# Kernel tuning notes

Hardware: AMD Instinct MI355X
Metric: run time of the kernel (lower is better)

## Reference

```python
import jax, jax.numpy as jnp
import numpy as np
import math

B, C, H, W = 16, 256, 56, 56
NH, WS = 8, 7            # num_heads, window_size
HID = 1024               # mlp_ratio * C

def _gelu(x):
    return jax.nn.gelu(x, approximate=False)  # torch nn.GELU default (erf)

def _ln(x, w, b, eps=1e-6):
    m = jnp.mean(x, -1, keepdims=True)
    v = jnp.mean((x - m) ** 2, -1, keepdims=True)
    return (x - m) * jax.lax.rsqrt(v + eps) * w + b

def _bn(x, g, b, eps=1e-5):
    # training-mode BatchNorm2d: batch statistics over (N,H,W)
    m = jnp.mean(x, (0, 2, 3), keepdims=True)
    v = jnp.mean((x - m) ** 2, (0, 2, 3), keepdims=True)
    return (x - m) * jax.lax.rsqrt(v + eps) * g[None, :, None, None] + b[None, :, None, None]

def _dwconv(x, w, b=None):
    y = jax.lax.conv_general_dilated(x, w, (1, 1), 'SAME',
                                     feature_group_count=x.shape[1],
                                     dimension_numbers=('NCHW', 'OIHW', 'NCHW'))
    if b is not None:
        y = y + b[None, :, None, None]
    return y

def _rel_pos_index(Wh, Ww):
    seq1 = np.arange(Wh) * (2 * Ww - 1)
    seq2 = np.arange(Ww)
    coords = (seq1[:, None] + seq2[None, :]).reshape(1, -1)
    idx = coords + coords.T               # [Wh*Ww, Wh*Ww]
    return jnp.asarray(np.ascontiguousarray(idx[:, ::-1]))  # flip(1)

REL_IDX = _rel_pos_index(WS, WS)  # [49, 49]

def setup_inputs():
    key = jax.random.key(0)
    ks = jax.random.split(key, 10)
    s = 0.02
    return dict(
        x=jax.random.normal(ks[0], (B, C, H, W), jnp.float32),
        ln1_w=jnp.ones((C,), jnp.float32), ln1_b=jnp.zeros((C,), jnp.float32),
        pos_w1=jax.random.normal(ks[1], (C, 1, 3, 3), jnp.float32) * s,
        pos_w2=jax.random.normal(ks[2], (C, 1, 3, 3), jnp.float32) * s,
        qkv_w=jax.random.normal(ks[3], (3 * C, C), jnp.float32) * s,
        qkv_b=jnp.zeros((3 * C,), jnp.float32),
        rpb=jax.random.normal(ks[4], ((2 * WS - 1) ** 2, NH), jnp.float32) * s,
        proj_w=jax.random.normal(ks[5], (C, C), jnp.float32) * s,
        proj_b=jnp.zeros((C,), jnp.float32),
        ln2_w=jnp.ones((C,), jnp.float32), ln2_b=jnp.zeros((C,), jnp.float32),
        fc1_w=jax.random.normal(ks[6], (HID, C), jnp.float32) * s,
        fc1_b=jnp.zeros((HID,), jnp.float32),
        bn1_g=jnp.ones((HID,), jnp.float32), bn1_b=jnp.zeros((HID,), jnp.float32),
        dw_w=jax.random.normal(ks[7], (HID, 1, 3, 3), jnp.float32) * s,
        dw_b=jnp.zeros((HID,), jnp.float32),
        bn2_g=jnp.ones((HID,), jnp.float32), bn2_b=jnp.zeros((HID,), jnp.float32),
        fc2_w=jax.random.normal(ks[8], (C, HID), jnp.float32) * s,
        fc2_b=jnp.zeros((C,), jnp.float32),
        bn3_g=jnp.ones((C,), jnp.float32), bn3_b=jnp.zeros((C,), jnp.float32),
    )

def _attention(xl, Hh, Ww_, pos_w1, pos_w2, qkv_w, qkv_b, rpb, proj_w, proj_b):
    Bq, N, Cc = xl.shape
    Wh = Ww = WS
    Hp = math.ceil(Hh / Wh) * Wh
    Wp = math.ceil(Ww_ / Ww) * Ww
    ph, pw = Hp - Hh, Wp - Ww_
    y = xl.reshape(Bq, Hh, Ww_, Cc)
    if ph or pw:
        y = jnp.pad(y, ((0, 0), (ph // 2, ph - ph // 2), (pw // 2, pw - pw // 2), (0, 0)))
    nWh, nWw = Hp // Wh, Wp // Ww
    # window partition -> [B*nWh*nWw, C, Wh, Ww]
    y = y.reshape(Bq, nWh, Wh, nWw, Ww, Cc).transpose(0, 1, 3, 2, 4, 5)
    xw = y.reshape(-1, Wh, Ww, Cc).transpose(0, 3, 1, 2)
    # per-window depthwise positional embedding: dw3x3 -> GELU -> dw3x3
    xw = xw + _dwconv(_gelu(_dwconv(xw, pos_w1)), pos_w2)
    t = xw.transpose(0, 2, 3, 1).reshape(-1, Wh * Ww, Cc)  # [Bw, 49, C]
    hd = Cc // NH
    qkv = (t @ qkv_w.T + qkv_b).reshape(-1, Wh * Ww, 3, NH, hd).transpose(2, 0, 3, 1, 4)
    q, k, v = qkv[0] * (hd ** -0.5), qkv[1], qkv[2]        # [Bw, NH, 49, hd]
    attn = jnp.einsum('bhnd,bhmd->bhnm', q, k)
    bias = rpb[REL_IDX.reshape(-1)].reshape(Wh * Ww, Wh * Ww, NH).transpose(2, 0, 1)
    attn = jax.nn.softmax(attn + bias[None], axis=-1)
    o = jnp.einsum('bhnm,bhmd->bhnd', attn, v).transpose(0, 2, 1, 3).reshape(-1, Wh * Ww, Cc)
    o = o @ proj_w.T + proj_b
    # window merge + crop padding
    o = o.reshape(Bq, nWh, nWw, Wh, Ww, Cc).transpose(0, 1, 3, 2, 4, 5).reshape(Bq, Hp, Wp, Cc)
    o = o[:, ph // 2:Hh + ph // 2, pw // 2:Ww_ + pw // 2]
    return o.reshape(Bq, N, Cc)

def _ffn(z_nlc, Hh, Ww_, fc1_w, fc1_b, bn1_g, bn1_b, dw_w, dw_b, bn2_g, bn2_b,
         fc2_w, fc2_b, bn3_g, bn3_b):
    Bq, N, Cc = z_nlc.shape
    z = z_nlc.transpose(0, 2, 1).reshape(Bq, Cc, Hh, Ww_)
    z = jnp.einsum('bchw,oc->bohw', z, fc1_w) + fc1_b[None, :, None, None]
    z = _gelu(_bn(z, bn1_g, bn1_b))
    z = _gelu(_bn(_dwconv(z, dw_w, dw_b), bn2_g, bn2_b))
    z = jnp.einsum('bchw,oc->bohw', z, fc2_w) + fc2_b[None, :, None, None]
    z = _gelu(_bn(z, bn3_g, bn3_b))
    return z.reshape(Bq, z.shape[1], Hh * Ww_).transpose(0, 2, 1)

def reference(x, ln1_w, ln1_b, pos_w1, pos_w2, qkv_w, qkv_b, rpb, proj_w, proj_b,
              ln2_w, ln2_b, fc1_w, fc1_b, bn1_g, bn1_b, dw_w, dw_b, bn2_g, bn2_b,
              fc2_w, fc2_b, bn3_g, bn3_b):
    Bq, Cc, Hh, Ww_ = x.shape
    xl = x.reshape(Bq, Cc, Hh * Ww_).transpose(0, 2, 1)  # NCHW -> NLC
    xl = xl + _attention(_ln(xl, ln1_w, ln1_b), Hh, Ww_,
                         pos_w1, pos_w2, qkv_w, qkv_b, rpb, proj_w, proj_b)
    xl = xl + _ffn(_ln(xl, ln2_w, ln2_b), Hh, Ww_,
                   fc1_w, fc1_b, bn1_g, bn1_b, dw_w, dw_b, bn2_g, bn2_b,
                   fc2_w, fc2_b, bn3_g, bn3_b)
    return xl.transpose(0, 2, 1).reshape(Bq, Cc, Hh, Ww_)
```

## Files before the change

kernel.cpp:

```cpp
#include <hip/hip_runtime.h>
#include <math.h>

#define BB 16
#define CC 256
#define HH 56
#define WW2 56
#define HWW 3136
#define NTOK 50176
#define NHD 8
#define HD 32
#define WSZ 7
#define WIN 49
#define NWIN 1024
#define HID 1024
#define C3 768

typedef __attribute__((ext_vector_type(8))) short bf16x8;
typedef __attribute__((ext_vector_type(4))) float f32x4;

__device__ __forceinline__ float gelu_f(float x) {
    return 0.5f * x * (1.0f + erff(x * 0.70710678118654752f));
}

__global__ __launch_bounds__(256) void k_nchw_to_tok(const float* __restrict__ x,
                                                     float* __restrict__ xl) {
    __shared__ float tile[32][33];
    int b = blockIdx.z;
    int p0 = blockIdx.x * 32, c0 = blockIdx.y * 32;
    int tx = threadIdx.x, ty = threadIdx.y;
    const float* xb = x + (size_t)b * CC * HWW;
    #pragma unroll
    for (int r = 0; r < 32; r += 8)
        tile[ty + r][tx] = xb[(size_t)(c0 + ty + r) * HWW + p0 + tx];
    __syncthreads();
    float* xlb = xl + (size_t)b * HWW * CC;
    #pragma unroll
    for (int r = 0; r < 32; r += 8)
        xlb[(size_t)(p0 + ty + r) * CC + c0 + tx] = tile[tx][ty + r];
}

__global__ __launch_bounds__(256) void k_tok_to_nchw(const float* __restrict__ zl,
                                                     float* __restrict__ out) {
    __shared__ float tile[32][33];
    int b = blockIdx.z;
    int p0 = blockIdx.x * 32, c0 = blockIdx.y * 32;
    int tx = threadIdx.x, ty = threadIdx.y;
    const float* zb = zl + (size_t)b * HWW * CC;
    #pragma unroll
    for (int r = 0; r < 32; r += 8)
        tile[ty + r][tx] = zb[(size_t)(p0 + ty + r) * CC + c0 + tx];
    __syncthreads();
    float* ob = out + (size_t)b * CC * HWW;
    #pragma unroll
    for (int r = 0; r < 32; r += 8)
        ob[(size_t)(c0 + ty + r) * HWW + p0 + tx] = tile[tx][ty + r];
}

__global__ __launch_bounds__(256) void k_ln(const float* __restrict__ in,
                                            const float* __restrict__ w,
                                            const float* __restrict__ bia,
                                            float* __restrict__ out) {
    size_t t = blockIdx.x;
    int c = threadIdx.x;
    float v = in[t * CC + c];
    float s = v, sq = v * v;
    #pragma unroll
    for (int off = 32; off; off >>= 1) {
        s += __shfl_xor(s, off);
        sq += __shfl_xor(sq, off);
    }
    __shared__ float red[8];
    int wid = c >> 6, lane = c & 63;
    if (lane == 0) { red[wid] = s; red[4 + wid] = sq; }
    __syncthreads();
    s = red[0] + red[1] + red[2] + red[3];
    sq = red[4] + red[5] + red[6] + red[7];
    float m = s * (1.0f / CC);
    float var = sq * (1.0f / CC) - m * m;
    float rs = rsqrtf(var + 1e-6f);
    out[t * CC + c] = (v - m) * rs * w[c] + bia[c];
}

__global__ __launch_bounds__(256) void k_posenc(const float* __restrict__ xln,
                                                const float* __restrict__ w1,
                                                const float* __restrict__ w2,
                                                float* __restrict__ tout) {
    int win = blockIdx.x;
    int c = threadIdx.x;
    int b = win >> 6, wh = (win >> 3) & 7, ww = win & 7;
    const float* base = xln + ((size_t)b * HWW) * CC + c;
    float v[49];
    #pragma unroll
    for (int r = 0; r < 7; r++)
        #pragma unroll
        for (int s = 0; s < 7; s++)
            v[r * 7 + s] = base[(size_t)((wh * 7 + r) * WW2 + ww * 7 + s) * CC];
    float k1w[9], k2w[9];
    #pragma unroll
    for (int k = 0; k < 9; k++) { k1w[k] = w1[c * 9 + k]; k2w[k] = w2[c * 9 + k]; }
    float g[49];
    #pragma unroll
    for (int r = 0; r < 7; r++)
        #pragma unroll
        for (int s = 0; s < 7; s++) {
            float acc = 0.f;
            #pragma unroll
            for (int kr = 0; kr < 3; kr++)
                #pragma unroll
                for (int ks = 0; ks < 3; ks++) {
                    int rr = r + kr - 1, ss = s + ks - 1;
                    if (rr >= 0 && rr < 7 && ss >= 0 && ss < 7)
                        acc += v[rr * 7 + ss] * k1w[kr * 3 + ks];
                }
            g[r * 7 + s] = gelu_f(acc);
        }
    float* outp = tout + (size_t)win * WIN * CC + c;
    #pragma unroll
    for (int r = 0; r < 7; r++)
        #pragma unroll
        for (int s = 0; s < 7; s++) {
            float acc = 0.f;
            #pragma unroll
            for (int kr = 0; kr < 3; kr++)
                #pragma unroll
                for (int ks = 0; ks < 3; ks++) {
                    int rr = r + kr - 1, ss = s + ks - 1;
                    if (rr >= 0 && rr < 7 && ss >= 0 && ss < 7)
                        acc += g[rr * 7 + ss] * k2w[kr * 3 + ks];
                }
            outp[(size_t)(r * 7 + s) * CC] = v[r * 7 + s] + acc;
        }
}

__device__ __forceinline__ void cvt_split4(float4 v, unsigned& h0, unsigned& h1,
                                           unsigned& l0, unsigned& l1) {
    unsigned ux = __float_as_uint(v.x), uy = __float_as_uint(v.y);
    unsigned uz = __float_as_uint(v.z), uw = __float_as_uint(v.w);
    unsigned hx = ux & 0xFFFF0000u, hy = uy & 0xFFFF0000u;
    unsigned hz = uz & 0xFFFF0000u, hw = uw & 0xFFFF0000u;
    float lx = v.x - __uint_as_float(hx);
    float ly = v.y - __uint_as_float(hy);
    float lz = v.z - __uint_as_float(hz);
    float lw = v.w - __uint_as_float(hw);
    h0 = (hx >> 16) | hy;
    h1 = (hz >> 16) | hw;
    l0 = (__float_as_uint(lx) >> 16) | (__float_as_uint(ly) & 0xFFFF0000u);
    l1 = (__float_as_uint(lz) >> 16) | (__float_as_uint(lw) & 0xFFFF0000u);
}

#define LDK 40
template <int EPI>
__global__ __launch_bounds__(256) void k_gemm_mfma(const float* __restrict__ A,
                                                   const float* __restrict__ Bw,
                                                   const float* __restrict__ bias,
                                                   float* __restrict__ Out,
                                                   float* __restrict__ resid,
                                                   int N, int K) {
    __shared__ __align__(16) unsigned short Ah[128 * LDK];
    __shared__ __align__(16) unsigned short Al[128 * LDK];
    __shared__ __align__(16) unsigned short Bh[128 * LDK];
    __shared__ __align__(16) unsigned short Bl[128 * LDK];
    const int tid = threadIdx.x;
    const int bm = blockIdx.y * 128;
    const int bn = blockIdx.x * 128;
    const int srow = tid >> 3;
    const int skf = (tid & 7) * 4;
    const int lane = tid & 63;
    const int wave = tid >> 6;
    const int wm = (wave & 1) * 64;
    const int wn = (wave >> 1) * 64;
    const int frow = lane & 15;
    const int fk = (lane >> 4) * 8;

    f32x4 acc[4][4] = {};

    for (int k0 = 0; k0 < K; k0 += 32) {
        if (k0) __syncthreads();
        #pragma unroll
        for (int h = 0; h < 4; ++h) {
            int row = srow + h * 32;
            float4 av = *reinterpret_cast<const float4*>(&A[(size_t)(bm + row) * K + k0 + skf]);
            float4 bv = *reinterpret_cast<const float4*>(&Bw[(size_t)(bn + row) * K + k0 + skf]);
            unsigned h0, h1, l0, l1;
            cvt_split4(av, h0, h1, l0, l1);
            *reinterpret_cast<uint2*>(&Ah[row * LDK + skf]) = make_uint2(h0, h1);
            *reinterpret_cast<uint2*>(&Al[row * LDK + skf]) = make_uint2(l0, l1);
            cvt_split4(bv, h0, h1, l0, l1);
            *reinterpret_cast<uint2*>(&Bh[row * LDK + skf]) = make_uint2(h0, h1);
            *reinterpret_cast<uint2*>(&Bl[row * LDK + skf]) = make_uint2(l0, l1);
        }
        __syncthreads();
        bf16x8 a_h[4], a_l[4], b_h[4], b_l[4];
        #pragma unroll
        for (int mi = 0; mi < 4; mi++) {
            int idx = (wm + mi * 16 + frow) * LDK + fk;
            a_h[mi] = *reinterpret_cast<const bf16x8*>(&Ah[idx]);
            a_l[mi] = *reinterpret_cast<const bf16x8*>(&Al[idx]);
        }
        #pragma unroll
        for (int nj = 0; nj < 4; nj++) {
            int idx = (wn + nj * 16 + frow) * LDK + fk;
            b_h[nj] = *reinterpret_cast<const bf16x8*>(&Bh[idx]);
            b_l[nj] = *reinterpret_cast<const bf16x8*>(&Bl[idx]);
        }
        #pragma unroll
        for (int mi = 0; mi < 4; mi++)
            #pragma unroll
            for (int nj = 0; nj < 4; nj++) {
                acc[mi][nj] = __builtin_amdgcn_mfma_f32_16x16x32_bf16(a_h[mi], b_h[nj], acc[mi][nj], 0, 0, 0);
                acc[mi][nj] = __builtin_amdgcn_mfma_f32_16x16x32_bf16(a_l[mi], b_h[nj], acc[mi][nj], 0, 0, 0);
                acc[mi][nj] = __builtin_amdgcn_mfma_f32_16x16x32_bf16(a_h[mi], b_l[nj], acc[mi][nj], 0, 0, 0);
            }
    }

    const int rbase = (lane >> 4) * 4;
    #pragma unroll
    for (int mi = 0; mi < 4; mi++) {
        #pragma unroll
        for (int nj = 0; nj < 4; nj++) {
            int gcol = bn + wn + nj * 16 + frow;
            float bval = bias[gcol];
            #pragma unroll
            for (int r = 0; r < 4; r++) {
                int grow = bm + wm + mi * 16 + rbase + r;
                float val = acc[mi][nj][r] + bval;
                if (EPI == 0) {
                    Out[(size_t)grow * N + gcol] = val;
                } else {
                    int win = grow / 49, ii = grow - win * 49;
                    int b = win >> 6, wh = (win >> 3) & 7, ww = win & 7;
                    int rr = ii / 7, ss = ii - rr * 7;
                    size_t tok = (size_t)b * HWW + (size_t)((wh * 7 + rr) * WW2 + ww * 7 + ss);
                    resid[tok * CC + gcol] += val;
                }
            }
        }
    }
}

__global__ __launch_bounds__(256) void k_attn(const float* __restrict__ qkv,
                                              const float* __restrict__ rpb,
                                              float* __restrict__ O) {
    __shared__ float qs[49][32], ks[49][32], vs[49][32];
    __shared__ float S[49][52];
    const int tid = threadIdx.x;
    const int win = blockIdx.x >> 3;
    const int head = blockIdx.x & 7;
    const float* base = qkv + (size_t)win * WIN * C3 + head * HD;
    for (int idx = tid; idx < WIN * HD; idx += 256) {
        int i = idx >> 5, d = idx & 31;
        const float* bp = base + (size_t)i * C3 + d;
        qs[i][d] = bp[0] * 0.17677669529663687f;
        ks[i][d] = bp[CC];
        vs[i][d] = bp[2 * CC];
    }
    __syncthreads();
    for (int idx = tid; idx < WIN * WIN; idx += 256) {
        int i = idx / 49, j = idx - i * 49;
        const float4* qp = reinterpret_cast<const float4*>(qs[i]);
        const float4* kp = reinterpret_cast<const float4*>(ks[j]);
        float acc = 0.f;
        #pragma unroll
        for (int d = 0; d < 8; d++) {
            float4 a = qp[d], b2 = kp[d];
            acc += a.x * b2.x + a.y * b2.y + a.z * b2.z + a.w * b2.w;
        }
        int ci = (i / 7) * 13 + (i % 7);
        int jr = 48 - j;
        int cj = (jr / 7) * 13 + (jr % 7);
        S[i][j] = acc + rpb[(ci + cj) * NHD + head];
    }
    __syncthreads();
    int wid = tid >> 6, lane = tid & 63;
    for (int row = wid; row < 49; row += 4) {
        float v = (lane < 49) ? S[row][lane] : -1e30f;
        float mx = v;
        #pragma unroll
        for (int off = 32; off; off >>= 1) mx = fmaxf(mx, __shfl_xor(mx, off));
        float e = (lane < 49) ? __expf(v - mx) : 0.f;
        float sm = e;
        #pragma unroll
        for (int off = 32; off; off >>= 1) sm += __shfl_xor(sm, off);
        if (lane < 49) S[row][lane] = e / sm;
    }
    __syncthreads();
    float* ob = O + (size_t)win * WIN * CC + head * HD;
    for (int idx = tid; idx < WIN * HD; idx += 256) {
        int i = idx >> 5, d = idx & 31;
        float acc = 0.f;
        #pragma unroll
        for (int j = 0; j < 49; j++) acc += S[i][j] * vs[j][d];
        ob[(size_t)i * CC + d] = acc;
    }
}

__global__ __launch_bounds__(256) void k_colstats(const float* __restrict__ Z,
                                                  float* __restrict__ sums, int nch) {
    int c = blockIdx.y * 256 + threadIdx.x;
    int t0 = blockIdx.x * 256;
    const float* zp = Z + (size_t)t0 * nch + c;
    float s = 0.f, sq = 0.f;
    for (int t = 0; t < 256; t++) {
        float v = zp[(size_t)t * nch];
        s += v; sq += v * v;
    }
    atomicAdd(&sums[c], s);
    atomicAdd(&sums[nch + c], sq);
}

__global__ void k_bnfin(const float* __restrict__ sums, const float* __restrict__ g,
                        const float* __restrict__ b, float* __restrict__ ss, int nch) {
    int c = blockIdx.x * 256 + threadIdx.x;
    if (c >= nch) return;
    float m = sums[c] * (1.0f / NTOK);
    float var = sums[nch + c] * (1.0f / NTOK) - m * m;
    float sc = rsqrtf(var + 1e-5f) * g[c];
    ss[c] = sc;
    ss[nch + c] = b[c] - m * sc;
}

__global__ __launch_bounds__(256) void k_act(float* __restrict__ Z,
                                             const float* __restrict__ ss,
                                             int nch, size_t total4) {
    size_t idx = (size_t)blockIdx.x * 256 + threadIdx.x;
    if (idx >= total4) return;
    float4 v = reinterpret_cast<float4*>(Z)[idx];
    int c0 = (int)((idx << 2) & (size_t)(nch - 1));
    v.x = gelu_f(v.x * ss[c0 + 0] + ss[nch + c0 + 0]);
    v.y = gelu_f(v.y * ss[c0 + 1] + ss[nch + c0 + 1]);
    v.z = gelu_f(v.z * ss[c0 + 2] + ss[nch + c0 + 2]);
    v.w = gelu_f(v.w * ss[c0 + 3] + ss[nch + c0 + 3]);
    reinterpret_cast<float4*>(Z)[idx] = v;
}

__global__ __launch_bounds__(256) void k_resfin(float* __restrict__ Z,
                                                const float* __restrict__ XL,
                                                const float* __restrict__ ss,
                                                size_t total4) {
    size_t idx = (size_t)blockIdx.x * 256 + threadIdx.x;
    if (idx >= total4) return;
    float4 v = reinterpret_cast<float4*>(Z)[idx];
    float4 xr = reinterpret_cast<const float4*>(XL)[idx];
    int c0 = (int)((idx << 2) & (size_t)(CC - 1));
    v.x = gelu_f(v.x * ss[c0 + 0] + ss[CC + c0 + 0]) + xr.x;
    v.y = gelu_f(v.y * ss[c0 + 1] + ss[CC + c0 + 1]) + xr.y;
    v.z = gelu_f(v.z * ss[c0 + 2] + ss[CC + c0 + 2]) + xr.z;
    v.w = gelu_f(v.w * ss[c0 + 3] + ss[CC + c0 + 3]) + xr.w;
    reinterpret_cast<float4*>(Z)[idx] = v;
}

__global__ __launch_bounds__(256) void k_dwconv_ip(float* __restrict__ Z,
                                                   const float* __restrict__ wt,
                                                   const float* __restrict__ bias) {
    __shared__ float rb[3][56][32];
    const int b  = blockIdx.x >> 5;
    const int c0 = (blockIdx.x & 31) * 32;
    const int tid = threadIdx.x;
    const int c = tid & 31, wg = tid >> 5;
    float* zb = Z + (size_t)b * HWW * HID + c0;
    float w9[9];
    #pragma unroll
    for (int k = 0; k < 9; k++) w9[k] = wt[(c0 + c) * 9 + k];
    const float bval = bias[c0 + c];

    for (int idx = tid; idx < 56 * 32; idx += 256) {
        int wcol = idx >> 5, ch = idx & 31;
        rb[0][wcol][ch] = zb[(size_t)(0 * 56 + wcol) * HID + ch];
        rb[1][wcol][ch] = zb[(size_t)(1 * 56 + wcol) * HID + ch];
    }
    __syncthreads();

    for (int h = 0; h < 56; ++h) {
        const int bm1 = (h + 2) % 3;
        const int b0  = h % 3;
        const int bp1 = (h + 1) % 3;
        float outv[7];
        #pragma unroll
        for (int i = 0; i < 7; i++) {
            int w = wg * 7 + i;
            float acc = bval;
            #pragma unroll
            for (int kr = 0; kr < 3; kr++) {
                int hh = h + kr - 1;
                if (hh < 0 || hh >= 56) continue;
                const float (*row)[32] = (kr == 0) ? rb[bm1] : (kr == 1 ? rb[b0] : rb[bp1]);
                #pragma unroll
                for (int ks = 0; ks < 3; ks++) {
                    int ww = w + ks - 1;
                    if (ww < 0 || ww >= 56) continue;
                    acc += row[ww][c] * w9[kr * 3 + ks];
                }
            }
            outv[i] = acc;
        }
        #pragma unroll
        for (int i = 0; i < 7; i++)
            zb[(size_t)(h * 56 + wg * 7 + i) * HID + c] = outv[i];
        __syncthreads();
        if (h + 2 < 56) {
            for (int idx = tid; idx < 56 * 32; idx += 256) {
                int wcol = idx >> 5, ch = idx & 31;
                rb[bm1][wcol][ch] = zb[(size_t)((h + 2) * 56 + wcol) * HID + ch];
            }
        }
        __syncthreads();
    }
}

__global__ __launch_bounds__(256) void k_zero(float* __restrict__ p, size_t n) {
    size_t i = (size_t)blockIdx.x * 256 + threadIdx.x;
    if (i < n) p[i] = 0.f;
}

extern "C" void kernel_launch(void* const* d_in, const int* in_sizes, int n_in,
                              void* d_out, int out_size, void* d_ws, size_t ws_size,
                              hipStream_t stream) {
    const float* x      = (const float*)d_in[0];
    const float* ln1_w  = (const float*)d_in[1];
    const float* ln1_b  = (const float*)d_in[2];
    const float* pos_w1 = (const float*)d_in[3];
    const float* pos_w2 = (const float*)d_in[4];
    const float* qkv_w  = (const float*)d_in[5];
    const float* qkv_b  = (const float*)d_in[6];
    const float* rpb    = (const float*)d_in[7];
    const float* proj_w = (const float*)d_in[8];
    const float* proj_b = (const float*)d_in[9];
    const float* ln2_w  = (const float*)d_in[10];
    const float* ln2_b  = (const float*)d_in[11];
    const float* fc1_w  = (const float*)d_in[12];
    const float* fc1_b  = (const float*)d_in[13];
    const float* bn1_g  = (const float*)d_in[14];
    const float* bn1_b  = (const float*)d_in[15];
    const float* dw_w   = (const float*)d_in[16];
    const float* dw_b   = (const float*)d_in[17];
    const float* bn2_g  = (const float*)d_in[18];
    const float* bn2_b  = (const float*)d_in[19];
    const float* fc2_w  = (const float*)d_in[20];
    const float* fc2_b  = (const float*)d_in[21];
    const float* bn3_g  = (const float*)d_in[22];
    const float* bn3_b  = (const float*)d_in[23];
    float* OUT = (float*)d_out;

    const size_t SMALL = (size_t)NTOK * CC;
    const size_t BIG   = (size_t)NTOK * HID;
    const size_t QKVF  = (size_t)NTOK * C3;
    const size_t NEED  = (SMALL + BIG + 8 * HID) * sizeof(float);

    if (ws_size < NEED) {
        k_zero<<<(unsigned)((SMALL + 255) / 256), 256, 0, stream>>>(OUT, SMALL);
        return;
    }

    float* ws = (float*)d_ws;
    float* XL   = ws;
    float* BIGR = XL + SMALL;
    float* SCR  = BIGR + QKVF;
    float* SUMS = BIGR + BIG;
    float* SS1  = SUMS + 2 * HID;
    float* SS2  = SS1 + 2 * HID;
    float* SS3  = SS2 + 2 * HID;

    dim3 tb(32, 8);
    dim3 tg(HWW / 32, CC / 32, BB);

    k_nchw_to_tok<<<tg, tb, 0, stream>>>(x, XL);
    k_ln<<<NTOK, 256, 0, stream>>>(XL, ln1_w, ln1_b, OUT);
    k_posenc<<<NWIN, 256, 0, stream>>>(OUT, pos_w1, pos_w2, SCR);
    k_gemm_mfma<0><<<dim3(C3 / 128, NTOK / 128), 256, 0, stream>>>(SCR, qkv_w, qkv_b, BIGR, nullptr, C3, CC);
    k_attn<<<NWIN * NHD, 256, 0, stream>>>(BIGR, rpb, OUT);
    k_gemm_mfma<1><<<dim3(CC / 128, NTOK / 128), 256, 0, stream>>>(OUT, proj_w, proj_b, nullptr, XL, CC, CC);
    k_ln<<<NTOK, 256, 0, stream>>>(XL, ln2_w, ln2_b, OUT);
    k_gemm_mfma<0><<<dim3(HID / 128, NTOK / 128), 256, 0, stream>>>(OUT, fc1_w, fc1_b, BIGR, nullptr, HID, CC);
    hipMemsetAsync(SUMS, 0, 2 * HID * sizeof(float), stream);
    k_colstats<<<dim3(NTOK / 256, HID / 256), 256, 0, stream>>>(BIGR, SUMS, HID);
    k_bnfin<<<HID / 256, 256, 0, stream>>>(SUMS, bn1_g, bn1_b, SS1, HID);
    k_act<<<(unsigned)(BIG / 4 / 256), 256, 0, stream>>>(BIGR, SS1, HID, BIG / 4);
    k_dwconv_ip<<<BB * 32, 256, 0, stream>>>(BIGR, dw_w, dw_b);
    hipMemsetAsync(SUMS, 0, 2 * HID * sizeof(float), stream);
    k_colstats<<<dim3(NTOK / 256, HID / 256), 256, 0, stream>>>(BIGR, SUMS, HID);
    k_bnfin<<<HID / 256, 256, 0, stream>>>(SUMS, bn2_g, bn2_b, SS2, HID);
    k_act<<<(unsigned)(BIG / 4 / 256), 256, 0, stream>>>(BIGR, SS2, HID, BIG / 4);
    k_gemm_mfma<0><<<dim3(CC / 128, NTOK / 128), 256, 0, stream>>>(BIGR, fc2_w, fc2_b, OUT, nullptr, CC, HID);
    hipMemsetAsync(SUMS, 0, 2 * CC * sizeof(float), stream);
    k_colstats<<<dim3(NTOK / 256, CC / 256), 256, 0, stream>>>(OUT, SUMS, CC);
    k_bnfin<<<1, 256, 0, stream>>>(SUMS, bn3_g, bn3_b, SS3, CC);
    k_resfin<<<(unsigned)(SMALL / 4 / 256), 256, 0, stream>>>(OUT, XL, SS3, SMALL / 4);
    k_tok_to_nchw<<<tg, tb, 0, stream>>>(OUT, XL);
    hipMemcpyAsync(OUT, XL, SMALL * sizeof(float), hipMemcpyDeviceToDevice, stream);
}
```

Measured before the change: 1.583 ms.

## Store FFN hidden activations in bf16 and fuse BN/GELU into dwconv and fc2 loads

```diff
diff --git a/kernel.cpp b/kernel.cpp
--- a/kernel.cpp
+++ b/kernel.cpp
@@ -17,9 +17,18 @@
 
 typedef __attribute__((ext_vector_type(8))) short bf16x8;
 typedef __attribute__((ext_vector_type(4))) float f32x4;
+typedef unsigned short u16;
 
 __device__ __forceinline__ float gelu_f(float x) {
     return 0.5f * x * (1.0f + erff(x * 0.70710678118654752f));
+}
+__device__ __forceinline__ float bf2f(u16 u) {
+    return __uint_as_float(((unsigned)u) << 16);
+}
+__device__ __forceinline__ u16 f2bf(float f) {
+    unsigned u = __float_as_uint(f);
+    u += 0x7FFFu + ((u >> 16) & 1u);
+    return (u16)(u >> 16);
 }
 
 __global__ __launch_bounds__(256) void k_nchw_to_tok(const float* __restrict__ x,
@@ -37,23 +46,6 @@
     #pragma unroll
     for (int r = 0; r < 32; r += 8)
         xlb[(size_t)(p0 + ty + r) * CC + c0 + tx] = tile[tx][ty + r];
-}
-
-__global__ __launch_bounds__(256) void k_tok_to_nchw(const float* __restrict__ zl,
-                                                     float* __restrict__ out) {
-    __shared__ float tile[32][33];
-    int b = blockIdx.z;
-    int p0 = blockIdx.x * 32, c0 = blockIdx.y * 32;
-    int tx = threadIdx.x, ty = threadIdx.y;
-    const float* zb = zl + (size_t)b * HWW * CC;
-    #pragma unroll
-    for (int r = 0; r < 32; r += 8)
-        tile[ty + r][tx] = zb[(size_t)(p0 + ty + r) * CC + c0 + tx];
-    __syncthreads();
-    float* ob = out + (size_t)b * CC * HWW;
-    #pragma unroll
-    for (int r = 0; r < 32; r += 8)
-        ob[(size_t)(c0 + ty + r) * HWW + p0 + tx] = tile[tx][ty + r];
 }
 
 __global__ __launch_bounds__(256) void k_ln(const float* __restrict__ in,
@@ -155,11 +147,12 @@
                                                    const float* __restrict__ bias,
                                                    float* __restrict__ Out,
                                                    float* __restrict__ resid,
+                                                   u16* __restrict__ Out16,
                                                    int N, int K) {
-    __shared__ __align__(16) unsigned short Ah[128 * LDK];
-    __shared__ __align__(16) unsigned short Al[128 * LDK];
-    __shared__ __align__(16) unsigned short Bh[128 * LDK];
-    __shared__ __align__(16) unsigned short Bl[128 * LDK];
+    __shared__ __align__(16) u16 Ah[128 * LDK];
+    __shared__ __align__(16) u16 Al[128 * LDK];
+    __shared__ __align__(16) u16 Bh[128 * LDK];
+    __shared__ __align__(16) u16 Bl[128 * LDK];
     const int tid = threadIdx.x;
     const int bm = blockIdx.y * 128;
     const int bn = blockIdx.x * 128;
@@ -226,16 +219,109 @@
                 float val = acc[mi][nj][r] + bval;
                 if (EPI == 0) {
                     Out[(size_t)grow * N + gcol] = val;
-                } else {
+                } else if (EPI == 1) {
                     int win = grow / 49, ii = grow - win * 49;
                     int b = win >> 6, wh = (win >> 3) & 7, ww = win & 7;
                     int rr = ii / 7, ss = ii - rr * 7;
                     size_t tok = (size_t)b * HWW + (size_t)((wh * 7 + rr) * WW2 + ww * 7 + ss);
                     resid[tok * CC + gcol] += val;
+                } else {
+                    Out16[(size_t)grow * N + gcol] = f2bf(val);
                 }
             }
         }
     }
+}
+
+__global__ __launch_bounds__(256) void k_gemm_a16(const u16* __restrict__ A16,
+                                                  const float* __restrict__ ss2,
+                                                  const float* __restrict__ Bw,
+                                                  const float* __restrict__ bias,
+                                                  float* __restrict__ Out,
+                                                  int N, int K) {
+    __shared__ __align__(16) u16 Ah[128 * LDK];
+    __shared__ __align__(16) u16 Bh[128 * LDK];
+    __shared__ __align__(16) u16 Bl[128 * LDK];
+    const int tid = threadIdx.x;
+    const int bm = blockIdx.y * 128;
+    const int bn = blockIdx.x * 128;
+    const int r2 = tid >> 2;
+    const int kh = (tid & 3) * 8;
+    const int srow = tid >> 3;
+    const int skf = (tid & 7) * 4;
+    const int lane = tid & 63;
+    const int wave = tid >> 6;
+    const int wm = (wave & 1) * 64;
+    const int wn = (wave >> 1) * 64;
+    const int frow = lane & 15;
+    const int fk = (lane >> 4) * 8;
+
+    f32x4 acc[4][4] = {};
+
+    for (int k0 = 0; k0 < K; k0 += 32) {
+        if (k0) __syncthreads();
+        #pragma unroll
+        for (int h = 0; h < 2; ++h) {
+            int row = r2 + h * 64;
+            uint4 av = *reinterpret_cast<const uint4*>(&A16[(size_t)(bm + row) * K + k0 + kh]);
+            const u16* ap = reinterpret_cast<const u16*>(&av);
+            float4 s0 = *reinterpret_cast<const float4*>(&ss2[k0 + kh]);
+            float4 s1 = *reinterpret_cast<const float4*>(&ss2[k0 + kh + 4]);
+            float4 t0 = *reinterpret_cast<const float4*>(&ss2[HID + k0 + kh]);
+            float4 t1 = *reinterpret_cast<const float4*>(&ss2[HID + k0 + kh + 4]);
+            u16 o8[8];
+            o8[0] = f2bf(gelu_f(bf2f(ap[0]) * s0.x + t0.x));
+            o8[1] = f2bf(gelu_f(bf2f(ap[1]) * s0.y + t0.y));
+            o8[2] = f2bf(gelu_f(bf2f(ap[2]) * s0.z + t0.z));
+            o8[3] = f2bf(gelu_f(bf2f(ap[3]) * s0.w + t0.w));
+            o8[4] = f2bf(gelu_f(bf2f(ap[4]) * s1.x + t1.x));
+            o8[5] = f2bf(gelu_f(bf2f(ap[5]) * s1.y + t1.y));
+            o8[6] = f2bf(gelu_f(bf2f(ap[6]) * s1.z + t1.z));
+            o8[7] = f2bf(gelu_f(bf2f(ap[7]) * s1.w + t1.w));
+            *reinterpret_cast<uint4*>(&Ah[row * LDK + kh]) = *reinterpret_cast<uint4*>(o8);
+        }
+        #pragma unroll
+        for (int h = 0; h < 4; ++h) {
+            int row = srow + h * 32;
+            float4 bv = *reinterpret_cast<const float4*>(&Bw[(size_t)(bn + row) * K + k0 + skf]);
+            unsigned h0, h1, l0, l1;
+            cvt_split4(bv, h0, h1, l0, l1);
+            *reinterpret_cast<uint2*>(&Bh[row * LDK + skf]) = make_uint2(h0, h1);
+            *reinterpret_cast<uint2*>(&Bl[row * LDK + skf]) = make_uint2(l0, l1);
+        }
+        __syncthreads();
+        bf16x8 a_h[4], b_h[4], b_l[4];
+        #pragma unroll
+        for (int mi = 0; mi < 4; mi++)
+            a_h[mi] = *reinterpret_cast<const bf16x8*>(&Ah[(wm + mi * 16 + frow) * LDK + fk]);
+        #pragma unroll
+        for (int nj = 0; nj < 4; nj++) {
+            int idx = (wn + nj * 16 + frow) * LDK + fk;
+            b_h[nj] = *reinterpret_cast<const bf16x8*>(&Bh[idx]);
+            b_l[nj] = *reinterpret_cast<const bf16x8*>(&Bl[idx]);
+        }
+        #pragma unroll
+        for (int mi = 0; mi < 4; mi++)
+            #pragma unroll
+            for (int nj = 0; nj < 4; nj++) {
+                acc[mi][nj] = __builtin_amdgcn_mfma_f32_16x16x32_bf16(a_h[mi], b_h[nj], acc[mi][nj], 0, 0, 0);
+                acc[mi][nj] = __builtin_amdgcn_mfma_f32_16x16x32_bf16(a_h[mi], b_l[nj], acc[mi][nj], 0, 0, 0);
+            }
+    }
+
+    const int rbase = (lane >> 4) * 4;
+    #pragma unroll
+    for (int mi = 0; mi < 4; mi++)
+        #pragma unroll
+        for (int nj = 0; nj < 4; nj++) {
+            int gcol = bn + wn + nj * 16 + frow;
+            float bval = bias[gcol];
+            #pragma unroll
+            for (int r = 0; r < 4; r++) {
+                int grow = bm + wm + mi * 16 + rbase + r;
+                Out[(size_t)grow * N + gcol] = acc[mi][nj][r] + bval;
+            }
+        }
 }
 
 __global__ __launch_bounds__(256) void k_attn(const float* __restrict__ qkv,
@@ -308,6 +394,20 @@
     atomicAdd(&sums[nch + c], sq);
 }
 
+__global__ __launch_bounds__(256) void k_colstats16(const u16* __restrict__ Z,
+                                                    float* __restrict__ sums, int nch) {
+    int c = blockIdx.y * 256 + threadIdx.x;
+    int t0 = blockIdx.x * 256;
+    const u16* zp = Z + (size_t)t0 * nch + c;
+    float s = 0.f, sq = 0.f;
+    for (int t = 0; t < 256; t++) {
+        float v = bf2f(zp[(size_t)t * nch]);
+        s += v; sq += v * v;
+    }
+    atomicAdd(&sums[c], s);
+    atomicAdd(&sums[nch + c], sq);
+}
+
 __global__ void k_bnfin(const float* __restrict__ sums, const float* __restrict__ g,
                         const float* __restrict__ b, float* __restrict__ ss, int nch) {
     int c = blockIdx.x * 256 + threadIdx.x;
@@ -319,91 +419,119 @@
     ss[nch + c] = b[c] - m * sc;
 }
 
-__global__ __launch_bounds__(256) void k_act(float* __restrict__ Z,
-                                             const float* __restrict__ ss,
-                                             int nch, size_t total4) {
-    size_t idx = (size_t)blockIdx.x * 256 + threadIdx.x;
-    if (idx >= total4) return;
-    float4 v = reinterpret_cast<float4*>(Z)[idx];
-    int c0 = (int)((idx << 2) & (size_t)(nch - 1));
-    v.x = gelu_f(v.x * ss[c0 + 0] + ss[nch + c0 + 0]);
-    v.y = gelu_f(v.y * ss[c0 + 1] + ss[nch + c0 + 1]);
-    v.z = gelu_f(v.z * ss[c0 + 2] + ss[nch + c0 + 2]);
-    v.w = gelu_f(v.w * ss[c0 + 3] + ss[nch + c0 + 3]);
-    reinterpret_cast<float4*>(Z)[idx] = v;
-}
-
-__global__ __launch_bounds__(256) void k_resfin(float* __restrict__ Z,
-                                                const float* __restrict__ XL,
-                                                const float* __restrict__ ss,
-                                                size_t total4) {
-    size_t idx = (size_t)blockIdx.x * 256 + threadIdx.x;
-    if (idx >= total4) return;
-    float4 v = reinterpret_cast<float4*>(Z)[idx];
-    float4 xr = reinterpret_cast<const float4*>(XL)[idx];
-    int c0 = (int)((idx << 2) & (size_t)(CC - 1));
-    v.x = gelu_f(v.x * ss[c0 + 0] + ss[CC + c0 + 0]) + xr.x;
-    v.y = gelu_f(v.y * ss[c0 + 1] + ss[CC + c0 + 1]) + xr.y;
-    v.z = gelu_f(v.z * ss[c0 + 2] + ss[CC + c0 + 2]) + xr.z;
-    v.w = gelu_f(v.w * ss[c0 + 3] + ss[CC + c0 + 3]) + xr.w;
-    reinterpret_cast<float4*>(Z)[idx] = v;
-}
-
-__global__ __launch_bounds__(256) void k_dwconv_ip(float* __restrict__ Z,
-                                                   const float* __restrict__ wt,
-                                                   const float* __restrict__ bias) {
-    __shared__ float rb[3][56][32];
-    const int b  = blockIdx.x >> 5;
-    const int c0 = (blockIdx.x & 31) * 32;
+__global__ __launch_bounds__(256) void k_dwconv_tok(const u16* __restrict__ Zin,
+                                                    const float* __restrict__ ss1,
+                                                    const float* __restrict__ wt,
+                                                    const float* __restrict__ bias,
+                                                    u16* __restrict__ Zout,
+                                                    float* __restrict__ sums2) {
+    __shared__ u16 sm[10][56][32];
+    __shared__ float rs[256], rq[256];
+    const int bx = blockIdx.x;
+    const int b = bx / 224;
+    const int rem = bx - b * 224;
+    const int band = rem >> 5;
+    const int chk = rem & 31;
+    const int c0 = chk * 32;
+    const int h0 = band * 8;
     const int tid = threadIdx.x;
-    const int c = tid & 31, wg = tid >> 5;
-    float* zb = Z + (size_t)b * HWW * HID + c0;
+
+    for (int idx = tid; idx < 10 * 56 * 4; idx += 256) {
+        int chunk = idx & 3;
+        int q = idx >> 2;
+        int row = q / 56;
+        int pix = q - row * 56;
+        int h = h0 - 1 + row;
+        u16 o8[8];
+        if (h < 0 || h >= HH) {
+            #pragma unroll
+            for (int j = 0; j < 8; j++) o8[j] = 0;
+        } else {
+            size_t off = ((size_t)(b * HWW + h * WW2 + pix)) * HID + c0 + chunk * 8;
+            uint4 av = *reinterpret_cast<const uint4*>(&Zin[off]);
+            const u16* ap = reinterpret_cast<const u16*>(&av);
+            #pragma unroll
+            for (int j = 0; j < 8; j++) {
+                int cc = c0 + chunk * 8 + j;
+                float v = bf2f(ap[j]);
+                o8[j] = f2bf(gelu_f(v * ss1[cc] + ss1[HID + cc]));
+            }
+        }
+        *reinterpret_cast<uint4*>(&sm[row][pix][chunk * 8]) = *reinterpret_cast<uint4*>(o8);
+    }
+    __syncthreads();
+
+    const int c = tid & 31;
+    const int wg = tid >> 5;
+    const int wbase = wg * 7;
     float w9[9];
     #pragma unroll
     for (int k = 0; k < 9; k++) w9[k] = wt[(c0 + c) * 9 + k];
     const float bval = bias[c0 + c];
-
-    for (int idx = tid; idx < 56 * 32; idx += 256) {
-        int wcol = idx >> 5, ch = idx & 31;
-        rb[0][wcol][ch] = zb[(size_t)(0 * 56 + wcol) * HID + ch];
-        rb[1][wcol][ch] = zb[(size_t)(1 * 56 + wcol) * HID + ch];
-    }
-    __syncthreads();
-
-    for (int h = 0; h < 56; ++h) {
-        const int bm1 = (h + 2) % 3;
-        const int b0  = h % 3;
-        const int bp1 = (h + 1) % 3;
-        float outv[7];
+    const bool lok = (wbase > 0);
+    const bool rok = (wbase + 7 < WW2);
+
+    float win[3][9];
+    #pragma unroll
+    for (int r = 0; r < 2; r++) {
+        win[r][0] = lok ? bf2f(sm[r][wbase - 1][c]) : 0.f;
+        #pragma unroll
+        for (int j = 0; j < 7; j++) win[r][1 + j] = bf2f(sm[r][wbase + j][c]);
+        win[r][8] = rok ? bf2f(sm[r][wbase + 7][c]) : 0.f;
+    }
+
+    float s = 0.f, sq = 0.f;
+    u16* zb = Zout + ((size_t)(b * HWW + h0 * WW2)) * HID + c0 + c;
+    #pragma unroll
+    for (int hh = 0; hh < 8; ++hh) {
+        const int rn = (hh + 2) % 3;
+        win[rn][0] = lok ? bf2f(sm[hh + 2][wbase - 1][c]) : 0.f;
+        #pragma unroll
+        for (int j = 0; j < 7; j++) win[rn][1 + j] = bf2f(sm[hh + 2][wbase + j][c]);
+        win[rn][8] = rok ? bf2f(sm[hh + 2][wbase + 7][c]) : 0.f;
+        const int r0 = hh % 3, r1 = (hh + 1) % 3, r2 = (hh + 2) % 3;
         #pragma unroll
         for (int i = 0; i < 7; i++) {
-            int w = wg * 7 + i;
             float acc = bval;
-            #pragma unroll
-            for (int kr = 0; kr < 3; kr++) {
-                int hh = h + kr - 1;
-                if (hh < 0 || hh >= 56) continue;
-                const float (*row)[32] = (kr == 0) ? rb[bm1] : (kr == 1 ? rb[b0] : rb[bp1]);
-                #pragma unroll
-                for (int ks = 0; ks < 3; ks++) {
-                    int ww = w + ks - 1;
-                    if (ww < 0 || ww >= 56) continue;
-                    acc += row[ww][c] * w9[kr * 3 + ks];
-                }
-            }
-            outv[i] = acc;
-        }
-        #pragma unroll
-        for (int i = 0; i < 7; i++)
-            zb[(size_t)(h * 56 + wg * 7 + i) * HID + c] = outv[i];
-        __syncthreads();
-        if (h + 2 < 56) {
-            for (int idx = tid; idx < 56 * 32; idx += 256) {
-                int wcol = idx >> 5, ch = idx & 31;
-                rb[bm1][wcol][ch] = zb[(size_t)((h + 2) * 56 + wcol) * HID + ch];
-            }
-        }
-        __syncthreads();
+            acc += win[r0][i] * w9[0] + win[r0][i + 1] * w9[1] + win[r0][i + 2] * w9[2];
+            acc += win[r1][i] * w9[3] + win[r1][i + 1] * w9[4] + win[r1][i + 2] * w9[5];
+            acc += win[r2][i] * w9[6] + win[r2][i + 1] * w9[7] + win[r2][i + 2] * w9[8];
+            zb[(size_t)(hh * WW2 + wbase + i) * HID] = f2bf(acc);
+            s += acc; sq += acc * acc;
+        }
+    }
+    rs[tid] = s; rq[tid] = sq;
+    __syncthreads();
+    if (tid < 32) {
+        float st = 0.f, qt = 0.f;
+        #pragma unroll
+        for (int g = 0; g < 8; g++) { st += rs[g * 32 + tid]; qt += rq[g * 32 + tid]; }
+        atomicAdd(&sums2[c0 + tid], st);
+        atomicAdd(&sums2[HID + c0 + tid], qt);
+    }
+}
+
+__global__ __launch_bounds__(256) void k_final(const float* __restrict__ Z3,
+                                               const float* __restrict__ XL,
+                                               const float* __restrict__ ss,
+                                               float* __restrict__ out) {
+    __shared__ float tile[32][33];
+    int b = blockIdx.z, p0 = blockIdx.x * 32, c0 = blockIdx.y * 32;
+    int tx = threadIdx.x, ty = threadIdx.y;
+    const float* zb = Z3 + (size_t)b * HWW * CC;
+    const float* xb = XL + (size_t)b * HWW * CC;
+    #pragma unroll
+    for (int r = 0; r < 32; r += 8) {
+        int p = p0 + ty + r, c = c0 + tx;
+        float v = zb[(size_t)p * CC + c];
+        tile[ty + r][tx] = gelu_f(v * ss[c] + ss[CC + c]) + xb[(size_t)p * CC + c];
+    }
+    __syncthreads();
+    float* ob = out + (size_t)b * CC * HWW;
+    #pragma unroll
+    for (int r = 0; r < 32; r += 8) {
+        int c = c0 + ty + r, p = p0 + tx;
+        ob[(size_t)c * HWW + p] = tile[tx][ty + r];
     }
 }
 
@@ -443,7 +571,6 @@
 
     const size_t SMALL = (size_t)NTOK * CC;
     const size_t BIG   = (size_t)NTOK * HID;
-    const size_t QKVF  = (size_t)NTOK * C3;
     const size_t NEED  = (SMALL + BIG + 8 * HID) * sizeof(float);
 
     if (ws_size < NEED) {
@@ -453,9 +580,13 @@
 
     float* ws = (float*)d_ws;
     float* XL   = ws;
-    float* BIGR = XL + SMALL;
-    float* SCR  = BIGR + QKVF;
-    float* SUMS = BIGR + BIG;
+    float* R    = XL + SMALL;
+    float* SCR  = R;
+    float* QKV  = R + SMALL;
+    u16*   H16A = (u16*)R;
+    u16*   H16B = H16A + BIG;
+    float* FR   = R;
+    float* SUMS = R + BIG;
     float* SS1  = SUMS + 2 * HID;
     float* SS2  = SS1 + 2 * HID;
     float* SS3  = SS2 + 2 * HID;
@@ -466,25 +597,21 @@
     k_nchw_to_tok<<<tg, tb, 0, stream>>>(x, XL);
     k_ln<<<NTOK, 256, 0, stream>>>(XL, ln1_w, ln1_b, OUT);
     k_posenc<<<NWIN, 256, 0, stream>>>(OUT, pos_w1, pos_w2, SCR);
-    k_gemm_mfma<0><<<dim3(C3 / 128, NTOK / 128), 256, 0, stream>>>(SCR, qkv_w, qkv_b, BIGR, nullptr, C3, CC);
-    k_attn<<<NWIN * NHD, 256, 0, stream>>>(BIGR, rpb, OUT);
-    k_gemm_mfma<1><<<dim3(CC / 128, NTOK / 128), 256, 0, stream>>>(OUT, proj_w, proj_b, nullptr, XL, CC, CC);
+    k_gemm_mfma<0><<<dim3(C3 / 128, NTOK / 128), 256, 0, stream>>>(SCR, qkv_w, qkv_b, QKV, nullptr, nullptr, C3, CC);
+    k_attn<<<NWIN * NHD, 256, 0, stream>>>(QKV, rpb, OUT);
+    k_gemm_mfma<1><<<dim3(CC / 128, NTOK / 128), 256, 0, stream>>>(OUT, proj_w, proj_b, nullptr, XL, nullptr, CC, CC);
     k_ln<<<NTOK, 256, 0, stream>>>(XL, ln2_w, ln2_b, OUT);
-    k_gemm_mfma<0><<<dim3(HID / 128, NTOK / 128), 256, 0, stream>>>(OUT, fc1_w, fc1_b, BIGR, nullptr, HID, CC);
+    k_gemm_mfma<2><<<dim3(HID / 128, NTOK / 128), 256, 0, stream>>>(OUT, fc1_w, fc1_b, nullptr, nullptr, H16A, HID, CC);
     hipMemsetAsync(SUMS, 0, 2 * HID * sizeof(float), stream);
-    k_colstats<<<dim3(NTOK / 256, HID / 256), 256, 0, stream>>>(BIGR, SUMS, HID);
+    k_colstats16<<<dim3(NTOK / 256, HID / 256), 256, 0, stream>>>(H16A, SUMS, HID);
     k_bnfin<<<HID / 256, 256, 0, stream>>>(SUMS, bn1_g, bn1_b, SS1, HID);
-    k_act<<<(unsigned)(BIG / 4 / 256), 256, 0, stream>>>(BIGR, SS1, HID, BIG / 4);
-    k_dwconv_ip<<<BB * 32, 256, 0, stream>>>(BIGR, dw_w, dw_b);
     hipMemsetAsync(SUMS, 0, 2 * HID * sizeof(float), stream);
-    k_colstats<<<dim3(NTOK / 256, HID / 256), 256, 0, stream>>>(BIGR, SUMS, HID);
+    k_dwconv_tok<<<BB * 7 * 32, 256, 0, stream>>>(H16A, SS1, dw_w, dw_b, H16B, SUMS);
     k_bnfin<<<HID / 256, 256, 0, stream>>>(SUMS, bn2_g, bn2_b, SS2, HID);
-    k_act<<<(unsigned)(BIG / 4 / 256), 256, 0, stream>>>(BIGR, SS2, HID, BIG / 4);
-    k_gemm_mfma<0><<<dim3(CC / 128, NTOK / 128), 256, 0, stream>>>(BIGR, fc2_w, fc2_b, OUT, nullptr, CC, HID);
+    k_gemm_a16<<<dim3(CC / 128, NTOK / 128), 256, 0, stream>>>(H16B, SS2, fc2_w, fc2_b, OUT, CC, HID);
     hipMemsetAsync(SUMS, 0, 2 * CC * sizeof(float), stream);
     k_colstats<<<dim3(NTOK / 256, CC / 256), 256, 0, stream>>>(OUT, SUMS, CC);
     k_bnfin<<<1, 256, 0, stream>>>(SUMS, bn3_g, bn3_b, SS3, CC);
-    k_resfin<<<(unsigned)(SMALL / 4 / 256), 256, 0, stream>>>(OUT, XL, SS3, SMALL / 4);
-    k_tok_to_nchw<<<tg, tb, 0, stream>>>(OUT, XL);
-    hipMemcpyAsync(OUT, XL, SMALL * sizeof(float), hipMemcpyDeviceToDevice, stream);
-}
+    k_final<<<tg, tb, 0, stream>>>(OUT, XL, SS3, FR);
+    hipMemcpyAsync(OUT, FR, SMALL * sizeof(float), hipMemcpyDeviceToDevice, stream);
+}
```

New measurement: 1.270 ms. 19.7% less time.
